# Kernel tuning notes

Hardware: AMD Instinct MI355X
Metric: run time of the kernel (lower is better)

The kernel has to match this reference:

```python
import jax, jax.numpy as jnp
import numpy as np

D_MODEL, D_INT, H = 1024, 64, 16
LAMBDA_INIT = 0.8
B, S = 2, 2048
LN_EPS = 1e-5


def setup_inputs() -> dict:
    key = jax.random.key(0)
    ks = jax.random.split(key, 12)
    sd = 0.02
    return {
        "x": jax.random.normal(ks[0], (B, S, D_MODEL), dtype=jnp.float32),
        "lambda_current": jnp.float32(0.5),
        "mask": jnp.ones((B, S), dtype=jnp.int32),
        # stacked per-head params (WQ1/WK1/WV; WQ2/WK2 are unused in source due to bug)
        "wq": sd * jax.random.normal(ks[1], (H, D_MODEL, D_INT), dtype=jnp.float32),
        "bq": sd * jax.random.normal(ks[2], (H, D_INT), dtype=jnp.float32),
        "wk": sd * jax.random.normal(ks[3], (H, D_MODEL, D_INT), dtype=jnp.float32),
        "bk": sd * jax.random.normal(ks[4], (H, D_INT), dtype=jnp.float32),
        "wv": sd * jax.random.normal(ks[5], (H, D_MODEL, 2 * D_INT), dtype=jnp.float32),
        "bv": sd * jax.random.normal(ks[6], (H, 2 * D_INT), dtype=jnp.float32),
        "wo": sd * jax.random.normal(ks[7], (2 * H * D_INT, D_MODEL), dtype=jnp.float32),
        "bo": sd * jax.random.normal(ks[8], (D_MODEL,), dtype=jnp.float32),
        "ln_g": jnp.ones((2 * D_INT,), dtype=jnp.float32),
        "ln_b": jnp.zeros((2 * D_INT,), dtype=jnp.float32),
    }


def reference(x, lambda_current, mask, wq, bq, wk, bk, wv, bv, wo, bo, ln_g, ln_b):
    b, s, d_model = x.shape
    scale = 1.0 / (d_model ** 0.5)  # source divides by sqrt(WQ1.in_features)
    # per-head projections: [H, B, S, d]
    Q = jnp.einsum('bsd,hdk->hbsk', x, wq) + bq[:, None, None, :]
    K = jnp.einsum('bsd,hdk->hbsk', x, wk) + bk[:, None, None, :]
    V = jnp.einsum('bsd,hdv->hbsv', x, wv) + bv[:, None, None, :]
    scores = jnp.einsum('hbsk,hbtk->hbst', Q, K) * scale
    scores = jnp.where(mask[None, :, None, :] == 0, -jnp.inf, scores)
    A1 = jax.nn.softmax(scores, axis=-1)
    # source bug: Q2/K2 reuse WQ1/WK1 => A2 == A1, so A = A1 - lambda*A2 = (1-lambda)*A1
    A = (1.0 - lambda_current) * A1
    out = jnp.einsum('hbst,hbtv->hbsv', A, V)  # [H,B,S,2*D_INT]
    # per-head LayerNorm (shared gamma/beta), then scale by (1 - lambda_init)
    mu = out.mean(-1, keepdims=True)
    var = out.var(-1, keepdims=True)
    out = (out - mu) / jnp.sqrt(var + LN_EPS) * ln_g + ln_b
    out = out * (1.0 - LAMBDA_INIT)
    cat = out.transpose(1, 2, 0, 3).reshape(b, s, -1)  # concat heads on feature dim
    res = cat @ wo + bo
    return (res, A)
```

## Files before the change

### kernel.cpp

```cpp
#include <hip/hip_runtime.h>
#include <hip/hip_bf16.h>

#define DM   1024
#define DI   64
#define H_   16
#define B_   2
#define S_   2048
#define NTOK 4096

typedef unsigned short u16;
typedef unsigned int u32;
typedef __attribute__((ext_vector_type(8))) short s16x8;
typedef __attribute__((ext_vector_type(4))) float f32x4;
typedef __attribute__((ext_vector_type(4))) unsigned int u32x4;
typedef __attribute__((ext_vector_type(4))) unsigned short u16x4;

#define AS1 __attribute__((address_space(1)))
#define AS3 __attribute__((address_space(3)))

static __device__ __forceinline__ u16 f2bf(float f) {
  unsigned int u = __builtin_bit_cast(unsigned int, f);
  unsigned int r = (u + 0x7fffu + ((u >> 16) & 1u)) >> 16;
  return (u16)r;
}

static __device__ __forceinline__ void gload_lds16(const u16* g, u16* l) {
  __builtin_amdgcn_global_load_lds((const AS1 u32*)(const void*)g,
                                   (AS3 u32*)(void*)l, 16, 0, 0);
}

static __device__ __forceinline__ void lds_barrier() {
  asm volatile("s_waitcnt lgkmcnt(0)\n\ts_barrier" ::: "memory");
}


__global__ void k_cvt_x(const float* __restrict__ in, u16* __restrict__ out) {
  int i = (blockIdx.x * 256 + threadIdx.x) * 4;
  float4 v = *(const float4*)&in[i];
  u16x4 o;
  o[0] = f2bf(v.x); o[1] = f2bf(v.y); o[2] = f2bf(v.z); o[3] = f2bf(v.w);
  *(u16x4*)&out[i] = o;
}

__global__ void k_small(const float* __restrict__ bq, const float* __restrict__ bk,
                        const float* __restrict__ bv, const int* __restrict__ mask,
                        float* __restrict__ bc, float* __restrict__ mbias,
                        u32* __restrict__ tmask) {
  int t = blockIdx.x * 256 + threadIdx.x;
  if (t < 1024) bc[t] = bq[t];
  else if (t < 2048) bc[t] = bk[t - 1024];
  else if (t < 4096) bc[t] = bv[t - 2048];
  else if (t < 8192) { int i = t - 4096; mbias[i] = mask[i] ? 0.f : -1e38f; }
  else if (t < 8256) {
    int tt = t - 8192;
    const int* mp = mask + (tt >> 5) * S_ + (tt & 31) * 64;
    int any0 = 0;
    for (int i = 0; i < 64; i++) any0 |= (mp[i] == 0);
    unsigned long long bal = __ballot(any0);
    if (tt == 0) { tmask[0] = (u32)bal; tmask[1] = (u32)(bal >> 32); }
  }
}

__global__ void k_tr_f2b(const float* __restrict__ in, u16* __restrict__ out, int R, int C) {
  __shared__ float t[32][33];
  const float* src = in + (size_t)blockIdx.z * R * C;
  u16* dst = out + (size_t)blockIdx.z * C * R;
  int r0 = blockIdx.y * 32, c0 = blockIdx.x * 32;
  for (int i = threadIdx.y; i < 32; i += 8)
    t[i][threadIdx.x] = src[(size_t)(r0 + i) * C + c0 + threadIdx.x];
  __syncthreads();
  for (int i = threadIdx.y; i < 32; i += 8)
    dst[(size_t)(c0 + i) * R + r0 + threadIdx.x] = f2bf(t[threadIdx.x][i]);
}

template<int MODE>
__global__ __launch_bounds__(256)
void k_gemm(const u16* __restrict__ A, const u16* __restrict__ Bt,
            const float* __restrict__ bias, int Kdim,
            u16* __restrict__ q_out, u16* __restrict__ k_out, u16* __restrict__ vt_out) {
  const int tid = threadIdx.x;
  const int l = tid & 63, w = tid >> 6;
  const int wm = w >> 1, wn = w & 1;
  const int g = l >> 4, lo = l & 15;
  const int m0 = blockIdx.y * 128, n0 = blockIdx.x * 128;
  __shared__ u16 As[128 * 64];
  __shared__ u16 Bs[128 * 64];
  f32x4 acc[4][4] = {};
  for (int kt = 0; kt < Kdim; kt += 64) {
    __syncthreads();
    for (int cid = tid; cid < 1024; cid += 256) {
      int r = cid >> 3, c = (cid & 7) * 8;
      gload_lds16(&A[(size_t)(m0 + r) * Kdim + kt + c], &As[cid * 8]);
      gload_lds16(&Bt[(size_t)(n0 + r) * Kdim + kt + c], &Bs[cid * 8]);
    }
    __syncthreads();
    for (int kc = 0; kc < 64; kc += 32) {
      s16x8 a[4], b[4];
      for (int i = 0; i < 4; i++)
        a[i] = *(const s16x8*)&As[(wm * 64 + i * 16 + lo) * 64 + kc + 8 * g];
      for (int i = 0; i < 4; i++)
        b[i] = *(const s16x8*)&Bs[(wn * 64 + i * 16 + lo) * 64 + kc + 8 * g];
      for (int mi = 0; mi < 4; mi++)
        for (int ni = 0; ni < 4; ni++)
          acc[mi][ni] = __builtin_amdgcn_mfma_f32_16x16x32_bf16(a[mi], b[ni], acc[mi][ni], 0, 0, 0);
    }
  }
  for (int mi = 0; mi < 4; mi++)
    for (int ni = 0; ni < 4; ni++)
      for (int j = 0; j < 4; j++) {
        int m = m0 + wm * 64 + mi * 16 + g * 4 + j;
        int n = n0 + wn * 64 + ni * 16 + lo;
        if (MODE == 0) {
          float v = acc[mi][ni][j] + bias[n];
          int bb = m >> 11, s = m & 2047;
          if (n < 1024) {
            int h = n >> 6, d = n & 63;
            q_out[(((size_t)h * B_ + bb) * S_ + s) * 64 + d] = f2bf(v);
          } else {
            int nn = n - 1024; int h = nn >> 6, d = nn & 63;
            k_out[(((size_t)h * B_ + bb) * S_ + s) * 64 + d] = f2bf(v);
          }
        } else {
          float v = acc[mi][ni][j] + bias[m];
          int h = m >> 7, d = m & 127;
          int bb = n >> 11, s = n & 2047;
          vt_out[(((size_t)h * B_ + bb) * 128 + d) * S_ + s] = f2bf(v);
        }
      }
}

__global__ __launch_bounds__(256)
void k_gemm64(const u16* __restrict__ A, const u16* __restrict__ Bt,
              const float* __restrict__ bias, int Kdim, float* __restrict__ res_out) {
  const int tid = threadIdx.x;
  const int l = tid & 63, w = tid >> 6;
  const int wm = w >> 1, wn = w & 1;
  const int g = l >> 4, lo = l & 15;
  const int m0 = blockIdx.y * 64, n0 = blockIdx.x * 128;
  __shared__ u16 As[64 * 64];
  __shared__ u16 Bs[128 * 64];
  f32x4 acc[2][4] = {};
  for (int kt = 0; kt < Kdim; kt += 64) {
    __syncthreads();
    for (int cid = tid; cid < 512; cid += 256) {
      int r = cid >> 3, c = (cid & 7) * 8;
      gload_lds16(&A[(size_t)(m0 + r) * Kdim + kt + c], &As[cid * 8]);
    }
    for (int cid = tid; cid < 1024; cid += 256) {
      int r = cid >> 3, c = (cid & 7) * 8;
      gload_lds16(&Bt[(size_t)(n0 + r) * Kdim + kt + c], &Bs[cid * 8]);
    }
    __syncthreads();
    for (int kc = 0; kc < 64; kc += 32) {
      s16x8 a[2], b[4];
      for (int i = 0; i < 2; i++)
        a[i] = *(const s16x8*)&As[(wm * 32 + i * 16 + lo) * 64 + kc + 8 * g];
      for (int i = 0; i < 4; i++)
        b[i] = *(const s16x8*)&Bs[(wn * 64 + i * 16 + lo) * 64 + kc + 8 * g];
      for (int mi = 0; mi < 2; mi++)
        for (int ni = 0; ni < 4; ni++)
          acc[mi][ni] = __builtin_amdgcn_mfma_f32_16x16x32_bf16(a[mi], b[ni], acc[mi][ni], 0, 0, 0);
    }
  }
  for (int mi = 0; mi < 2; mi++)
    for (int ni = 0; ni < 4; ni++)
      for (int j = 0; j < 4; j++) {
        int m = m0 + wm * 32 + mi * 16 + g * 4 + j;
        int n = n0 + wn * 64 + ni * 16 + lo;
        res_out[(size_t)m * 1024 + n] = acc[mi][ni][j] + bias[n];
      }
}

__global__ __launch_bounds__(256, 4)
void k_attn(const u16* __restrict__ Qb, const u16* __restrict__ Kb,
            const u16* __restrict__ Vtb, const float* __restrict__ mbias,
            const u32* __restrict__ tmask, const float* __restrict__ lam_p,
            const float* __restrict__ ln_g, const float* __restrict__ ln_b,
            float* __restrict__ A_out, u16* __restrict__ cat) {
  const int tid = threadIdx.x, l = tid & 63, w = tid >> 6;
  const int g = l >> 4, lo = l & 15;
  const int bid = blockIdx.x;
  const int xcd = bid & 7, idx = bid >> 3;
  const int hb = xcd * 4 + (idx >> 5);
  const int s0 = (idx & 31) * 64;
  const int b = hb & 1, h = hb >> 1;
  const float scale2 = 0.03125f * 1.44269504f;
  const float pfac = 1.0f - lam_p[0];
  const u32 tm = tmask[b];

  __shared__ __align__(16) u16 Ks[64 * 72];
  __shared__ __align__(16) u16 Vs[128 * 72];
  __shared__ __align__(16) u16 Ps[4][16 * 72];

  const u16* Qhb = Qb + (size_t)hb * S_ * 64;
  const u16* Khb = Kb + (size_t)hb * S_ * 64;
  const u16* Vthb = Vtb + (size_t)hb * 128 * S_;
  const float* mb = mbias + (size_t)b * S_;

  const int q = s0 + w * 16 + lo;
  const s16x8 q0 = *(const s16x8*)&Qhb[(size_t)q * 64 + 8 * g];
  const s16x8 q1 = *(const s16x8*)&Qhb[(size_t)q * 64 + 32 + 8 * g];
  float* Arow = A_out + ((size_t)hb * S_ + q) * S_;

  const int kr = tid >> 3, kc8 = (tid & 7) * 8;

  {
    *(u32x4*)&Ks[kr * 72 + kc8] = *(const u32x4*)&Khb[(size_t)kr * 64 + kc8];
    int cid = tid + 256; int r = cid >> 3, c = (cid & 7) * 8;
    *(u32x4*)&Ks[r * 72 + c] = *(const u32x4*)&Khb[(size_t)r * 64 + c];
  }
  __syncthreads();
  f32x4 psv = {};
  for (int t = 0; t < 32; t++) {
    const u16* rbuf = (t & 1) ? Vs : Ks;
    u16* wbuf = (t & 1) ? Ks : Vs;
    const int kt = t * 64;
    const int ktn = (kt + 64) & (S_ - 1);
    const bool mskt = (tm >> t) & 1;
    u32x4 kreg0 = *(const u32x4*)&Khb[(size_t)(ktn + kr) * 64 + kc8];
    u32x4 kreg1 = *(const u32x4*)&Khb[(size_t)(ktn + kr + 32) * 64 + kc8];
#pragma unroll
    for (int nf = 0; nf < 4; nf++) {
      s16x8 k0 = *(const s16x8*)&rbuf[(nf * 16 + lo) * 72 + 8 * g];
      s16x8 k1 = *(const s16x8*)&rbuf[(nf * 16 + lo) * 72 + 32 + 8 * g];
      f32x4 z = {};
      z = __builtin_amdgcn_mfma_f32_16x16x32_bf16(k0, q0, z, 0, 0, 0);
      z = __builtin_amdgcn_mfma_f32_16x16x32_bf16(k1, q1, z, 0, 0, 0);
      f32x4 m4 = {};
      if (mskt) m4 = *(const f32x4*)&mb[kt + nf * 16 + g * 4];
      psv[0] += __builtin_exp2f(z[0] * scale2 + m4[0]);
      psv[1] += __builtin_exp2f(z[1] * scale2 + m4[1]);
      psv[2] += __builtin_exp2f(z[2] * scale2 + m4[2]);
      psv[3] += __builtin_exp2f(z[3] * scale2 + m4[3]);
    }
    *(u32x4*)&wbuf[kr * 72 + kc8] = kreg0;
    *(u32x4*)&wbuf[(kr + 32) * 72 + kc8] = kreg1;
    __syncthreads();
  }
  float ps = (psv[0] + psv[1]) + (psv[2] + psv[3]);
  ps += __shfl_xor(ps, 16, 64);
  ps += __shfl_xor(ps, 32, 64);
  const float rinv = pfac / ps;

#pragma unroll
  for (int i = 0; i < 4; i++) {
    int cid = tid + i * 256;
    int r = cid >> 3, c = (cid & 7) * 8;
    *(u32x4*)&Vs[r * 72 + c] = *(const u32x4*)&Vthb[(size_t)r * S_ + c];
  }
  __syncthreads();

  f32x4 o[8] = {};
  for (int t = 0; t < 32; t++) {
    const int kt = t * 64;
    const bool pre = (t < 31);
    const bool mskt = (tm >> t) & 1;
    u32x4 kreg0, kreg1, vreg[4];
    if (pre) {
      const int ktn = kt + 64;
      kreg0 = *(const u32x4*)&Khb[(size_t)(ktn + kr) * 64 + kc8];
      kreg1 = *(const u32x4*)&Khb[(size_t)(ktn + kr + 32) * 64 + kc8];
#pragma unroll
      for (int i = 0; i < 4; i++) {
        int cid = tid + i * 256;
        vreg[i] = *(const u32x4*)&Vthb[(size_t)(cid >> 3) * S_ + ktn + (cid & 7) * 8];
      }
    }
    f32x4 z[4];
#pragma unroll
    for (int nf = 0; nf < 4; nf++) {
      s16x8 k0 = *(const s16x8*)&Ks[(nf * 16 + lo) * 72 + 8 * g];
      s16x8 k1 = *(const s16x8*)&Ks[(nf * 16 + lo) * 72 + 32 + 8 * g];
      f32x4 zz = {};
      zz = __builtin_amdgcn_mfma_f32_16x16x32_bf16(k0, q0, zz, 0, 0, 0);
      z[nf] = __builtin_amdgcn_mfma_f32_16x16x32_bf16(k1, q1, zz, 0, 0, 0);
    }
#pragma unroll
    for (int nf = 0; nf < 4; nf++) {
      f32x4 m4 = {};
      if (mskt) m4 = *(const f32x4*)&mb[kt + nf * 16 + g * 4];
      f32x4 p4;
      p4[0] = __builtin_exp2f(z[nf][0] * scale2 + m4[0]) * rinv;
      p4[1] = __builtin_exp2f(z[nf][1] * scale2 + m4[1]) * rinv;
      p4[2] = __builtin_exp2f(z[nf][2] * scale2 + m4[2]) * rinv;
      p4[3] = __builtin_exp2f(z[nf][3] * scale2 + m4[3]) * rinv;
      __builtin_nontemporal_store(p4, (f32x4*)&Arow[kt + nf * 16 + g * 4]);
      u16x4 pb;
      pb[0] = f2bf(p4[0]); pb[1] = f2bf(p4[1]);
      pb[2] = f2bf(p4[2]); pb[3] = f2bf(p4[3]);
      *(u16x4*)&Ps[w][lo * 72 + nf * 16 + g * 4] = pb;
    }
#pragma unroll
    for (int kc = 0; kc < 2; kc++) {
      s16x8 pa = *(const s16x8*)&Ps[w][lo * 72 + kc * 32 + 8 * g];
#pragma unroll
      for (int vf = 0; vf < 8; vf++) {
        s16x8 bv = *(const s16x8*)&Vs[(vf * 16 + lo) * 72 + kc * 32 + 8 * g];
        o[vf] = __builtin_amdgcn_mfma_f32_16x16x32_bf16(pa, bv, o[vf], 0, 0, 0);
      }
    }
    lds_barrier();
    if (pre) {
      *(u32x4*)&Ks[kr * 72 + kc8] = kreg0;
      *(u32x4*)&Ks[(kr + 32) * 72 + kc8] = kreg1;
#pragma unroll
      for (int i = 0; i < 4; i++) {
        int cid = tid + i * 256;
        *(u32x4*)&Vs[(cid >> 3) * 72 + (cid & 7) * 8] = vreg[i];
      }
    }
    lds_barrier();
  }

#pragma unroll
  for (int j = 0; j < 4; j++) {
    float sum = 0.f, sq = 0.f;
#pragma unroll
    for (int vf = 0; vf < 8; vf++) { float xv = o[vf][j]; sum += xv; sq += xv * xv; }
    for (int msk = 1; msk < 16; msk <<= 1) {
      sum += __shfl_xor(sum, msk, 64);
      sq += __shfl_xor(sq, msk, 64);
    }
    float mean = sum * (1.f / 128.f);
    float var = sq * (1.f / 128.f) - mean * mean;
    float rstd = rsqrtf(var + 1e-5f);
    int s = s0 + w * 16 + g * 4 + j;
    u16* cp = cat + ((size_t)(b * S_ + s)) * 2048 + h * 128;
#pragma unroll
    for (int vf = 0; vf < 8; vf++) {
      int c = vf * 16 + lo;
      float y = (o[vf][j] - mean) * rstd * ln_g[c] + ln_b[c];
      cp[c] = f2bf(y * 0.2f);
    }
  }
}


extern "C" void kernel_launch(void* const* d_in, const int* in_sizes, int n_in,
                              void* d_out, int out_size, void* d_ws, size_t ws_size,
                              hipStream_t stream) {
  const float* x    = (const float*)d_in[0];
  const float* lam  = (const float*)d_in[1];
  const int*   mask = (const int*)d_in[2];
  const float* wq   = (const float*)d_in[3];
  const float* bq   = (const float*)d_in[4];
  const float* wk   = (const float*)d_in[5];
  const float* bk   = (const float*)d_in[6];
  const float* wv   = (const float*)d_in[7];
  const float* bv   = (const float*)d_in[8];
  const float* wo   = (const float*)d_in[9];
  const float* bo   = (const float*)d_in[10];
  const float* lng  = (const float*)d_in[11];
  const float* lnb  = (const float*)d_in[12];

  float* res = (float*)d_out;
  float* A   = res + (size_t)NTOK * DM;

  char* ws = (char*)d_ws;
  size_t off = 0;
  auto alloc = [&](size_t bytes) {
    void* p = ws + off;
    off += (bytes + 255) & ~(size_t)255;
    return p;
  };
  u16*   xb    = (u16*)  alloc((size_t)NTOK * DM * 2);
  u16*   Wct   = (u16*)  alloc((size_t)4096 * 1024 * 2);
  float* bc    = (float*)alloc(4096 * 4);
  float* mbias = (float*)alloc(4096 * 4);
  u32*   tmask = (u32*)  alloc(2 * 4);
  u16*   wot   = (u16*)  alloc((size_t)1024 * 2048 * 2);
  u16*   Qb    = (u16*)  alloc((size_t)32 * S_ * 64 * 2);
  u16*   Kb2   = (u16*)  alloc((size_t)32 * S_ * 64 * 2);
  u16*   Vtb   = (u16*)  alloc((size_t)32 * S_ * 128 * 2);
  u16*   catb  = (u16*)ws;

  k_cvt_x<<<4096, 256, 0, stream>>>(x, xb);
  k_small<<<33, 256, 0, stream>>>(bq, bk, bv, mask, bc, mbias, tmask);
  k_tr_f2b<<<dim3(2, 32, 16), dim3(32, 8), 0, stream>>>(wq, Wct, 1024, 64);
  k_tr_f2b<<<dim3(2, 32, 16), dim3(32, 8), 0, stream>>>(wk, Wct + 1024 * 1024, 1024, 64);
  k_tr_f2b<<<dim3(4, 32, 16), dim3(32, 8), 0, stream>>>(wv, Wct + 2048 * 1024, 1024, 128);
  k_tr_f2b<<<dim3(32, 64, 1), dim3(32, 8), 0, stream>>>(wo, wot, 2048, 1024);
  k_gemm<0><<<dim3(16, 32), 256, 0, stream>>>(xb, Wct, bc, 1024, Qb, Kb2, nullptr);
  k_gemm<2><<<dim3(32, 16), 256, 0, stream>>>(Wct + (size_t)2048 * 1024, xb, bc + 2048,
                                              1024, nullptr, nullptr, Vtb);
  k_attn<<<dim3(1024), 256, 0, stream>>>(Qb, Kb2, Vtb, mbias, tmask, lam, lng, lnb, A, catb);
  k_gemm64<<<dim3(8, 64), 256, 0, stream>>>(catb, wot, bo, 2048, res);
}
```

Measured before the change: 349.8 us.

## Split softmax denominator pass into separate split-K kernel before attention

Moves the first pass of the two-pass softmax, which sums exp(scores) per row, out of the attention kernel into a new kernel. The new kernel splits the key range into two halves and uses double-buffered LDS with a prefetch guard. The attention kernel then reads the two partial sums from a workspace buffer and goes straight to the P·V pass. This doubles the grid for the denominator pass and should raise occupancy, at the cost of an extra launch, a small workspace round trip, and recomputing the QK products.

Measured after the change: 394.5 us. 1.13x slower.

```diff
diff --git a/kernel.cpp b/kernel.cpp
--- a/kernel.cpp
+++ b/kernel.cpp
@@ -171,12 +171,85 @@
       }
 }
 
+__global__ __launch_bounds__(256, 6)
+void k_den(const u16* __restrict__ Qb, const u16* __restrict__ Kb,
+           const float* __restrict__ mbias, const u32* __restrict__ tmask,
+           float* __restrict__ den) {
+  const int tid = threadIdx.x, l = tid & 63, w = tid >> 6;
+  const int g = l >> 4, lo = l & 15;
+  const int bid = blockIdx.x;
+  const int xcd = bid & 7, idx = bid >> 3;
+  const int hb = xcd * 4 + (idx >> 6);
+  const int rem = idx & 63;
+  const int s0 = (rem >> 1) * 64;
+  const int half = rem & 1;
+  const int b = hb & 1;
+  const float scale2 = 0.03125f * 1.44269504f;
+  const u32 tm = tmask[b];
+
+  __shared__ __align__(16) u16 Ks[2][64 * 72];
+
+  const u16* Qhb = Qb + (size_t)hb * S_ * 64;
+  const u16* Khb = Kb + (size_t)hb * S_ * 64 + (size_t)half * 1024 * 64;
+  const float* mb = mbias + (size_t)b * S_ + half * 1024;
+
+  const int q = s0 + w * 16 + lo;
+  const s16x8 q0 = *(const s16x8*)&Qhb[(size_t)q * 64 + 8 * g];
+  const s16x8 q1 = *(const s16x8*)&Qhb[(size_t)q * 64 + 32 + 8 * g];
+
+  const int kr = tid >> 3, kc8 = (tid & 7) * 8;
+
+  {
+    *(u32x4*)&Ks[0][kr * 72 + kc8] = *(const u32x4*)&Khb[(size_t)kr * 64 + kc8];
+    int cid = tid + 256; int r = cid >> 3, c = (cid & 7) * 8;
+    *(u32x4*)&Ks[0][r * 72 + c] = *(const u32x4*)&Khb[(size_t)r * 64 + c];
+  }
+  __syncthreads();
+  f32x4 psv = {};
+  for (int t = 0; t < 16; t++) {
+    const int buf = t & 1;
+    const int kt = t * 64;
+    const bool pre = (t < 15);
+    const bool mskt = (tm >> (half * 16 + t)) & 1;
+    u32x4 kreg0, kreg1;
+    if (pre) {
+      const int ktn = kt + 64;
+      kreg0 = *(const u32x4*)&Khb[(size_t)(ktn + kr) * 64 + kc8];
+      kreg1 = *(const u32x4*)&Khb[(size_t)(ktn + kr + 32) * 64 + kc8];
+    }
+#pragma unroll
+    for (int nf = 0; nf < 4; nf++) {
+      s16x8 k0 = *(const s16x8*)&Ks[buf][(nf * 16 + lo) * 72 + 8 * g];
+      s16x8 k1 = *(const s16x8*)&Ks[buf][(nf * 16 + lo) * 72 + 32 + 8 * g];
+      f32x4 z = {};
+      z = __builtin_amdgcn_mfma_f32_16x16x32_bf16(k0, q0, z, 0, 0, 0);
+      z = __builtin_amdgcn_mfma_f32_16x16x32_bf16(k1, q1, z, 0, 0, 0);
+      f32x4 m4 = {};
+      if (mskt) m4 = *(const f32x4*)&mb[kt + nf * 16 + g * 4];
+      psv[0] += __builtin_exp2f(z[0] * scale2 + m4[0]);
+      psv[1] += __builtin_exp2f(z[1] * scale2 + m4[1]);
+      psv[2] += __builtin_exp2f(z[2] * scale2 + m4[2]);
+      psv[3] += __builtin_exp2f(z[3] * scale2 + m4[3]);
+    }
+    if (pre) {
+      *(u32x4*)&Ks[buf ^ 1][kr * 72 + kc8] = kreg0;
+      *(u32x4*)&Ks[buf ^ 1][(kr + 32) * 72 + kc8] = kreg1;
+    }
+    lds_barrier();
+  }
+  float ps = (psv[0] + psv[1]) + (psv[2] + psv[3]);
+  ps += __shfl_xor(ps, 16, 64);
+  ps += __shfl_xor(ps, 32, 64);
+  if (g == 0) den[(size_t)half * 32 * S_ + (size_t)hb * S_ + q] = ps;
+}
+
 __global__ __launch_bounds__(256, 4)
 void k_attn(const u16* __restrict__ Qb, const u16* __restrict__ Kb,
             const u16* __restrict__ Vtb, const float* __restrict__ mbias,
-            const u32* __restrict__ tmask, const float* __restrict__ lam_p,
-            const float* __restrict__ ln_g, const float* __restrict__ ln_b,
-            float* __restrict__ A_out, u16* __restrict__ cat) {
+            const u32* __restrict__ tmask, const float* __restrict__ den,
+            const float* __restrict__ lam_p, const float* __restrict__ ln_g,
+            const float* __restrict__ ln_b, float* __restrict__ A_out,
+            u16* __restrict__ cat) {
   const int tid = threadIdx.x, l = tid & 63, w = tid >> 6;
   const int g = l >> 4, lo = l & 15;
   const int bid = blockIdx.x;
@@ -202,6 +275,10 @@
   const s16x8 q1 = *(const s16x8*)&Qhb[(size_t)q * 64 + 32 + 8 * g];
   float* Arow = A_out + ((size_t)hb * S_ + q) * S_;
 
+  const float d0 = den[(size_t)hb * S_ + q];
+  const float d1 = den[(size_t)32 * S_ + (size_t)hb * S_ + q];
+  const float rinv = pfac / (d0 + d1);
+
   const int kr = tid >> 3, kc8 = (tid & 7) * 8;
 
   {
@@ -209,39 +286,6 @@
     int cid = tid + 256; int r = cid >> 3, c = (cid & 7) * 8;
     *(u32x4*)&Ks[r * 72 + c] = *(const u32x4*)&Khb[(size_t)r * 64 + c];
   }
-  __syncthreads();
-  f32x4 psv = {};
-  for (int t = 0; t < 32; t++) {
-    const u16* rbuf = (t & 1) ? Vs : Ks;
-    u16* wbuf = (t & 1) ? Ks : Vs;
-    const int kt = t * 64;
-    const int ktn = (kt + 64) & (S_ - 1);
-    const bool mskt = (tm >> t) & 1;
-    u32x4 kreg0 = *(const u32x4*)&Khb[(size_t)(ktn + kr) * 64 + kc8];
-    u32x4 kreg1 = *(const u32x4*)&Khb[(size_t)(ktn + kr + 32) * 64 + kc8];
-#pragma unroll
-    for (int nf = 0; nf < 4; nf++) {
-      s16x8 k0 = *(const s16x8*)&rbuf[(nf * 16 + lo) * 72 + 8 * g];
-      s16x8 k1 = *(const s16x8*)&rbuf[(nf * 16 + lo) * 72 + 32 + 8 * g];
-      f32x4 z = {};
-      z = __builtin_amdgcn_mfma_f32_16x16x32_bf16(k0, q0, z, 0, 0, 0);
-      z = __builtin_amdgcn_mfma_f32_16x16x32_bf16(k1, q1, z, 0, 0, 0);
-      f32x4 m4 = {};
-      if (mskt) m4 = *(const f32x4*)&mb[kt + nf * 16 + g * 4];
-      psv[0] += __builtin_exp2f(z[0] * scale2 + m4[0]);
-      psv[1] += __builtin_exp2f(z[1] * scale2 + m4[1]);
-      psv[2] += __builtin_exp2f(z[2] * scale2 + m4[2]);
-      psv[3] += __builtin_exp2f(z[3] * scale2 + m4[3]);
-    }
-    *(u32x4*)&wbuf[kr * 72 + kc8] = kreg0;
-    *(u32x4*)&wbuf[(kr + 32) * 72 + kc8] = kreg1;
-    __syncthreads();
-  }
-  float ps = (psv[0] + psv[1]) + (psv[2] + psv[3]);
-  ps += __shfl_xor(ps, 16, 64);
-  ps += __shfl_xor(ps, 32, 64);
-  const float rinv = pfac / ps;
-
 #pragma unroll
   for (int i = 0; i < 4; i++) {
     int cid = tid + i * 256;
@@ -368,6 +412,7 @@
   float* bc    = (float*)alloc(4096 * 4);
   float* mbias = (float*)alloc(4096 * 4);
   u32*   tmask = (u32*)  alloc(2 * 4);
+  float* den   = (float*)alloc((size_t)2 * 32 * S_ * 4);
   u16*   wot   = (u16*)  alloc((size_t)1024 * 2048 * 2);
   u16*   Qb    = (u16*)  alloc((size_t)32 * S_ * 64 * 2);
   u16*   Kb2   = (u16*)  alloc((size_t)32 * S_ * 64 * 2);
@@ -383,6 +428,7 @@
   k_gemm<0><<<dim3(16, 32), 256, 0, stream>>>(xb, Wct, bc, 1024, Qb, Kb2, nullptr);
   k_gemm<2><<<dim3(32, 16), 256, 0, stream>>>(Wct + (size_t)2048 * 1024, xb, bc + 2048,
                                               1024, nullptr, nullptr, Vtb);
-  k_attn<<<dim3(1024), 256, 0, stream>>>(Qb, Kb2, Vtb, mbias, tmask, lam, lng, lnb, A, catb);
+  k_den<<<dim3(2048), 256, 0, stream>>>(Qb, Kb2, mbias, tmask, den);
+  k_attn<<<dim3(1024), 256, 0, stream>>>(Qb, Kb2, Vtb, mbias, tmask, den, lam, lng, lnb, A, catb);
   k_gemm64<<<dim3(8, 64), 256, 0, stream>>>(catb, wot, bo, 2048, res);
 }
```
